# Optimization experiments

Measured on AMD Instinct MI355X. Metric: run time of the kernel, lower is better.

Reference implementation:

```python
import jax, jax.numpy as jnp
import numpy as np

B, T, D, H = 4, 2048, 1024, 16
HD = D // H  # 64
NEG = -np.finfo(np.float32).max


def setup_inputs() -> dict:
    key = jax.random.key(0)
    ks = jax.random.split(key, 9)
    s = 1.0 / np.sqrt(D)
    return {
        "x": jax.random.normal(ks[0], (B, T, D), jnp.float32),
        "wq": jax.random.normal(ks[1], (D, D), jnp.float32) * s,
        "bq": jax.random.normal(ks[2], (D,), jnp.float32) * 0.02,
        "wk": jax.random.normal(ks[3], (D, D), jnp.float32) * s,
        "bk": jax.random.normal(ks[4], (D,), jnp.float32) * 0.02,
        "wv": jax.random.normal(ks[5], (D, D), jnp.float32) * s,
        "bv": jax.random.normal(ks[6], (D,), jnp.float32) * 0.02,
        "wo": jax.random.normal(ks[7], (D, D), jnp.float32) * s,
        "bo": jax.random.normal(ks[8], (D,), jnp.float32) * 0.02,
    }


def reference(x, wq, bq, wk, bk, wv, bv, wo, bo):
    b, t, d = x.shape
    # separate Q, K, V projections, reshape to (B, H, T, HD)
    def proj(w, bias):
        y = x @ w + bias
        return y.reshape(b, t, H, HD).transpose(0, 2, 1, 3)
    q = proj(wq, bq)
    k = proj(wk, bk)
    v = proj(wv, bv)
    scale = 1.0 / np.sqrt(HD).astype(np.float32)
    scores = jnp.einsum("bhqd,bhkd->bhqk", q, k) * scale  # (B,H,T,T)
    # causal mask: -max_float on strictly upper triangle (matches source)
    mask = jnp.triu(jnp.full((t, t), NEG, jnp.float32), k=1)
    attn = jax.nn.softmax(scores + mask, axis=-1)
    out = jnp.einsum("bhqk,bhkd->bhqd", attn, v)
    out = out.transpose(0, 2, 1, 3).reshape(b, t, d)
    return out @ wo + bo
```

## Files before the change

kernel.cpp:

```cpp
#include <hip/hip_runtime.h>

typedef __bf16 bf16x8 __attribute__((ext_vector_type(8)));
typedef float f32x4 __attribute__((ext_vector_type(4)));

#define B_ 4
#define T_ 2048
#define D_ 1024
#define H_ 16
#define HD_ 64
#define M_ 8192
#define QSCALE 0.1803368801111204f

__device__ __forceinline__ ushort f2b(float f) {
  union { float f; unsigned u; } v; v.f = f;
  unsigned u = v.u;
  return (ushort)((u + 0x7FFFu + ((u >> 16) & 1u)) >> 16);
}

__device__ __forceinline__ unsigned pkbf(float a, float b) {
  union { float f; unsigned u; } va, vb; va.f = a; vb.f = b;
  return __builtin_amdgcn_perm(vb.u + 0x8000u, va.u + 0x8000u, 0x07060302u);
}

__device__ __forceinline__ void gll16(const void* g, void* l) {
  __builtin_amdgcn_global_load_lds(
      (const __attribute__((address_space(1))) unsigned*)g,
      (__attribute__((address_space(3))) unsigned*)l, 16, 0, 0);
}

__global__ __launch_bounds__(256) void cast_x_kernel(const float* __restrict__ x,
                                                     ushort* __restrict__ xb) {
  int idx = blockIdx.x * 256 + threadIdx.x;
  float4 v = ((const float4*)x)[idx];
  ushort4 o;
  o.x = f2b(v.x); o.y = f2b(v.y); o.z = f2b(v.z); o.w = f2b(v.w);
  ((ushort4*)xb)[idx] = o;
}

__global__ __launch_bounds__(256) void transpose_w_kernel(
    const float* __restrict__ wq, const float* __restrict__ wk,
    const float* __restrict__ wv, const float* __restrict__ wo,
    ushort* __restrict__ wt_qkv, ushort* __restrict__ wt_o) {
  __shared__ float tile[32][33];
  int z = blockIdx.z;
  const float* src = (z == 0) ? wq : (z == 1) ? wk : (z == 2) ? wv : wo;
  ushort* dst = (z < 3) ? (wt_qkv + (size_t)z * D_ * D_) : wt_o;
  int n0 = blockIdx.x * 32, k0 = blockIdx.y * 32;
  int tx = threadIdx.x & 31, ty = threadIdx.x >> 5;
  for (int i = 0; i < 4; i++) {
    int r = ty + i * 8;
    tile[r][tx] = src[(size_t)(k0 + r) * D_ + n0 + tx];
  }
  __syncthreads();
  for (int i = 0; i < 4; i++) {
    int r = ty + i * 8;
    dst[(size_t)(n0 + r) * D_ + k0 + tx] = f2b(tile[tx][r]);
  }
}

__global__ __launch_bounds__(256) void gemm_kernel(
    const ushort* __restrict__ A, const ushort* __restrict__ Bt, int mode,
    const float* __restrict__ bias_q, const float* __restrict__ bias_k,
    const float* __restrict__ bias_v,
    ushort* __restrict__ qb, ushort* __restrict__ kb, ushort* __restrict__ vtb,
    float* __restrict__ outf) {
  __shared__ ushort As[2][128][64];
  __shared__ ushort Bs[2][128][64];
  int tid = threadIdx.x;
  int wave = tid >> 6, lane = tid & 63, lrow = lane >> 4, lcol = lane & 15;
  int m0 = blockIdx.y * 128, n0 = blockIdx.x * 128;
  int wm = (wave & 1) * 64, wn = (wave >> 1) * 64;

  int rb = tid >> 3;
  int dc = tid & 7;
  int scv = dc ^ (rb & 7);
  const ushort* aBase = A + (size_t)(m0 + rb) * D_ + scv * 8;
  const ushort* bBase = Bt + (size_t)(n0 + rb) * D_ + scv * 8;

  f32x4 zero = {0.f, 0.f, 0.f, 0.f};
  f32x4 acc[4][4];
  for (int i = 0; i < 4; i++)
    for (int j = 0; j < 4; j++) acc[i][j] = zero;

  int swz = lcol & 7;

  auto stage = [&](int buf, int k) {
#pragma unroll
    for (int g = 0; g < 4; g++) {
      gll16(aBase + (size_t)(32 * g) * D_ + k, &As[buf][0][0] + tid * 8 + g * 2048);
      gll16(bBase + (size_t)(32 * g) * D_ + k, &Bs[buf][0][0] + tid * 8 + g * 2048);
    }
  };

  stage(0, 0);

  for (int k0 = 0; k0 < D_; k0 += 64) {
    int cur = (k0 >> 6) & 1, nxt = cur ^ 1;
    __syncthreads();
    if (k0 + 64 < D_) stage(nxt, k0 + 64);

    for (int ks = 0; ks < 2; ks++) {
      bf16x8 af[4], bf[4];
      int ch = ((ks * 4 + lrow) ^ swz) * 8;
      for (int mt = 0; mt < 4; mt++)
        af[mt] = *(const bf16x8*)&As[cur][wm + mt * 16 + lcol][ch];
      for (int nt = 0; nt < 4; nt++)
        bf[nt] = *(const bf16x8*)&Bs[cur][wn + nt * 16 + lcol][ch];
      for (int mt = 0; mt < 4; mt++)
        for (int nt = 0; nt < 4; nt++)
          acc[mt][nt] = __builtin_amdgcn_mfma_f32_16x16x32_bf16(
              af[mt], bf[nt], acc[mt][nt], 0, 0, 0);
    }
  }

  if (mode == 0) {
    int proj = n0 >> 10;
    const float* bias = (proj == 0) ? bias_q : (proj == 1) ? bias_k : bias_v;
    for (int mt = 0; mt < 4; mt++) {
      int gm0 = m0 + wm + mt * 16 + lrow * 4;
      int b = gm0 >> 11, tp = gm0 & 2047;
      for (int nt = 0; nt < 4; nt++) {
        int gn = n0 + wn + nt * 16 + lcol;
        int inner = gn & 1023;
        int h = inner >> 6, hd = inner & 63;
        float bv = bias[inner];
        if (proj == 0) {
          size_t base = ((size_t)(b * H_ + h) * T_ + tp) * HD_ + hd;
          for (int r = 0; r < 4; r++)
            qb[base + (size_t)r * HD_] = f2b((acc[mt][nt][r] + bv) * QSCALE);
        } else if (proj == 1) {
          size_t base = ((size_t)(b * H_ + h) * T_ + tp) * HD_ + hd;
          for (int r = 0; r < 4; r++)
            kb[base + (size_t)r * HD_] = f2b(acc[mt][nt][r] + bv);
        } else {
          ushort4 pk;
          pk.x = f2b(acc[mt][nt][0] + bv);
          pk.y = f2b(acc[mt][nt][1] + bv);
          pk.z = f2b(acc[mt][nt][2] + bv);
          pk.w = f2b(acc[mt][nt][3] + bv);
          *(ushort4*)&vtb[((size_t)(b * H_ + h) * HD_ + hd) * T_ + tp] = pk;
        }
      }
    }
  } else {
    for (int mt = 0; mt < 4; mt++) {
      int gm0 = m0 + wm + mt * 16 + lrow * 4;
      for (int nt = 0; nt < 4; nt++) {
        int gn = n0 + wn + nt * 16 + lcol;
        float bv = bias_q[gn];
        for (int r = 0; r < 4; r++)
          outf[(size_t)(gm0 + r) * D_ + gn] = acc[mt][nt][r] + bv;
      }
    }
  }
}

__global__ __launch_bounds__(256) void flash_kernel(
    const ushort* __restrict__ qb, const ushort* __restrict__ kb,
    const ushort* __restrict__ vtb, ushort* __restrict__ ob) {
  __shared__ ushort Ks[64][72];
  __shared__ ushort Vs[64][72];
  __shared__ ushort Ps[4][16][72];
  int tid = threadIdx.x;
  int wave = tid >> 6, lane = tid & 63, lrow = lane >> 4, lcol = lane & 15;

  int bid = blockIdx.x + (blockIdx.y << 5);
  int xcd = bid & 7;
  int slot = bid >> 3;
  int bh = xcd * 8 + (slot >> 5);
  int qtile = 31 - (slot & 31);
  int b = bh >> 4, h = bh & 15;
  const ushort* qh = qb + (size_t)bh * T_ * HD_;
  const ushort* kh = kb + (size_t)bh * T_ * HD_;
  const ushort* vh = vtb + (size_t)bh * HD_ * T_;

  int r0 = tid >> 3, cb0 = (tid & 7) * 8;
  uint4 kr0 = *(const uint4*)&kh[(size_t)r0 * HD_ + cb0];
  uint4 kr1 = *(const uint4*)&kh[(size_t)(r0 + 32) * HD_ + cb0];
  uint4 vr0 = *(const uint4*)&vh[(size_t)r0 * T_ + cb0];
  uint4 vr1 = *(const uint4*)&vh[(size_t)(r0 + 32) * T_ + cb0];

  bf16x8 af1;
  {
    __bf16 ov = (__bf16)((lcol == 0) ? 1.0f : 0.0f);
    for (int i = 0; i < 8; i++) af1[i] = ov;
  }

  f32x4 zero = {0.f, 0.f, 0.f, 0.f};

  int q0w = qtile * 64 + wave * 16;
  bf16x8 qf[2];
  for (int ks = 0; ks < 2; ks++)
    qf[ks] = *(const bf16x8*)&qh[(size_t)(q0w + lcol) * HD_ + ks * 32 + lrow * 8];

  f32x4 accO[4];
  f32x4 accI;
  accI = zero;
  for (int mt = 0; mt < 4; mt++) accO[mt] = zero;

  for (int j = 0; j <= qtile; j++) {
    __syncthreads();
    *(uint4*)&Ks[r0][cb0] = kr0;
    *(uint4*)&Ks[r0 + 32][cb0] = kr1;
    *(uint4*)&Vs[r0][cb0] = vr0;
    *(uint4*)&Vs[r0 + 32][cb0] = vr1;
    __syncthreads();

    if (j < qtile) {
      int jn = j + 1;
      kr0 = *(const uint4*)&kh[(size_t)(jn * 64 + r0) * HD_ + cb0];
      kr1 = *(const uint4*)&kh[(size_t)(jn * 64 + r0 + 32) * HD_ + cb0];
      vr0 = *(const uint4*)&vh[(size_t)r0 * T_ + jn * 64 + cb0];
      vr1 = *(const uint4*)&vh[(size_t)(r0 + 32) * T_ + jn * 64 + cb0];
    }

    f32x4 st[4];
    for (int mt = 0; mt < 4; mt++) st[mt] = zero;
    for (int ks = 0; ks < 2; ks++)
      for (int mt = 0; mt < 4; mt++) {
        bf16x8 kf = *(const bf16x8*)&Ks[mt * 16 + lcol][ks * 32 + lrow * 8];
        st[mt] = __builtin_amdgcn_mfma_f32_16x16x32_bf16(kf, qf[ks], st[mt], 0, 0, 0);
      }

    if (j == qtile) {
      int q_g = q0w + lcol;
      for (int mt = 0; mt < 4; mt++)
        for (int r = 0; r < 4; r++) {
          int kv_g = j * 64 + mt * 16 + lrow * 4 + r;
          if (kv_g > q_g) st[mt][r] = -1e30f;
        }
    }

    for (int mt = 0; mt < 4; mt++)
      for (int r = 0; r < 4; r++)
        st[mt][r] = __builtin_amdgcn_exp2f(st[mt][r]);

    for (int mt = 0; mt < 4; mt++) {
      uint2 pk;
      pk.x = pkbf(st[mt][0], st[mt][1]);
      pk.y = pkbf(st[mt][2], st[mt][3]);
      *(uint2*)&Ps[wave][lcol][mt * 16 + lrow * 4] = pk;
    }

    for (int ks = 0; ks < 2; ks++) {
      bf16x8 pf = *(const bf16x8*)&Ps[wave][lcol][ks * 32 + lrow * 8];
      accI = __builtin_amdgcn_mfma_f32_16x16x32_bf16(af1, pf, accI, 0, 0, 0);
      for (int mt = 0; mt < 4; mt++) {
        bf16x8 vf = *(const bf16x8*)&Vs[mt * 16 + lcol][ks * 32 + lrow * 8];
        accO[mt] = __builtin_amdgcn_mfma_f32_16x16x32_bf16(vf, pf, accO[mt], 0, 0, 0);
      }
    }
  }

  float lsum = __shfl(accI[0], lcol);
  float linv = 1.f / lsum;
  int t = q0w + lcol;
  size_t base = ((size_t)b * T_ + t) * D_ + h * HD_;
  for (int mt = 0; mt < 4; mt++) {
    uint2 pk;
    pk.x = pkbf(accO[mt][0] * linv, accO[mt][1] * linv);
    pk.y = pkbf(accO[mt][2] * linv, accO[mt][3] * linv);
    *(uint2*)&ob[base + mt * 16 + lrow * 4] = pk;
  }
}

extern "C" void kernel_launch(void* const* d_in, const int* in_sizes, int n_in,
                              void* d_out, int out_size, void* d_ws, size_t ws_size,
                              hipStream_t stream) {
  (void)in_sizes; (void)n_in; (void)out_size; (void)ws_size;
  const float* x  = (const float*)d_in[0];
  const float* wq = (const float*)d_in[1];
  const float* bq = (const float*)d_in[2];
  const float* wk = (const float*)d_in[3];
  const float* bk = (const float*)d_in[4];
  const float* wv = (const float*)d_in[5];
  const float* bv = (const float*)d_in[6];
  const float* wo = (const float*)d_in[7];
  const float* bo = (const float*)d_in[8];
  float* out = (float*)d_out;

  char* ws = (char*)d_ws;
  ushort* xb     = (ushort*)(ws);
  ushort* wt_qkv = (ushort*)(ws + 16777216);
  ushort* wt_o   = (ushort*)(ws + 23068672);
  ushort* qb     = (ushort*)(ws + 25165824);
  ushort* kb     = (ushort*)(ws + 41943040);
  ushort* vtb    = (ushort*)(ws + 58720256);
  ushort* ob     = (ushort*)(ws + 75497472);

  cast_x_kernel<<<8192, 256, 0, stream>>>(x, xb);
  transpose_w_kernel<<<dim3(32, 32, 4), 256, 0, stream>>>(wq, wk, wv, wo, wt_qkv, wt_o);
  gemm_kernel<<<dim3(24, 64), 256, 0, stream>>>(xb, wt_qkv, 0, bq, bk, bv, qb, kb, vtb, nullptr);
  flash_kernel<<<dim3(32, 64), 256, 0, stream>>>(qb, kb, vtb, ob);
  gemm_kernel<<<dim3(8, 64), 256, 0, stream>>>(ob, wt_o, 1, bo, nullptr, nullptr,
                                               nullptr, nullptr, nullptr, out);
}
```

Before: 268.1 us.

## Double flash query tile per block, add XCD-aware GEMM remap and MFMA priority

The flash kernel now handles 128 query rows per block, with each wave owning 32 rows in two 16-row halves. Every K/V tile loaded into LDS is therefore reused across twice as many queries, and the grid is halved. LDS row padding changes to 80 and s_setprio is raised around the MFMA sections. The GEMM kernel remaps block IDs so consecutive work tiles land on the same XCD, aiming for better L2 locality. The cost is more registers per thread, which may reduce occupancy, and coarser causal load balance.

```diff
diff --git a/kernel.cpp b/kernel.cpp
--- a/kernel.cpp
+++ b/kernel.cpp
@@ -68,7 +68,12 @@
   __shared__ ushort Bs[2][128][64];
   int tid = threadIdx.x;
   int wave = tid >> 6, lane = tid & 63, lrow = lane >> 4, lcol = lane & 15;
-  int m0 = blockIdx.y * 128, n0 = blockIdx.x * 128;
+
+  int gx = gridDim.x;
+  int nwg = gx * gridDim.y;
+  int orig = blockIdx.x + gx * blockIdx.y;
+  int work = (orig & 7) * (nwg >> 3) + (orig >> 3);
+  int m0 = (work / gx) * 128, n0 = (work % gx) * 128;
   int wm = (wave & 1) * 64, wn = (wave >> 1) * 64;
 
   int rb = tid >> 3;
@@ -158,19 +163,19 @@
 __global__ __launch_bounds__(256) void flash_kernel(
     const ushort* __restrict__ qb, const ushort* __restrict__ kb,
     const ushort* __restrict__ vtb, ushort* __restrict__ ob) {
-  __shared__ ushort Ks[64][72];
-  __shared__ ushort Vs[64][72];
-  __shared__ ushort Ps[4][16][72];
+  __shared__ ushort Ks[64][80];
+  __shared__ ushort Vs[64][80];
+  __shared__ ushort Ps[4][32][80];
   int tid = threadIdx.x;
   int wave = tid >> 6, lane = tid & 63, lrow = lane >> 4, lcol = lane & 15;
 
-  int bid = blockIdx.x + (blockIdx.y << 5);
+  int bid = blockIdx.x + (blockIdx.y << 4);
   int xcd = bid & 7;
   int slot = bid >> 3;
-  int bh = xcd * 8 + (slot >> 5);
-  int qtile = 31 - (slot & 31);
+  int bh = xcd * 8 + (slot >> 4);
+  int qblk = 15 - (slot & 15);
   int b = bh >> 4, h = bh & 15;
-  const ushort* qh = qb + (size_t)bh * T_ * HD_;
+  const ushort* qp = qb + (size_t)bh * T_ * HD_;
   const ushort* kh = kb + (size_t)bh * T_ * HD_;
   const ushort* vh = vtb + (size_t)bh * HD_ * T_;
 
@@ -188,17 +193,25 @@
 
   f32x4 zero = {0.f, 0.f, 0.f, 0.f};
 
-  int q0w = qtile * 64 + wave * 16;
-  bf16x8 qf[2];
-  for (int ks = 0; ks < 2; ks++)
-    qf[ks] = *(const bf16x8*)&qh[(size_t)(q0w + lcol) * HD_ + ks * 32 + lrow * 8];
-
-  f32x4 accO[4];
-  f32x4 accI;
-  accI = zero;
-  for (int mt = 0; mt < 4; mt++) accO[mt] = zero;
-
-  for (int j = 0; j <= qtile; j++) {
+  int q0w = qblk * 128 + wave * 32;
+  bf16x8 qf[2][2];
+#pragma unroll
+  for (int qh = 0; qh < 2; qh++)
+#pragma unroll
+    for (int ks = 0; ks < 2; ks++)
+      qf[qh][ks] = *(const bf16x8*)&qp[(size_t)(q0w + qh * 16 + lcol) * HD_ +
+                                       ks * 32 + lrow * 8];
+
+  f32x4 accO[2][4];
+  f32x4 accS[2];
+#pragma unroll
+  for (int qh = 0; qh < 2; qh++) {
+    accS[qh] = zero;
+    for (int mt = 0; mt < 4; mt++) accO[qh][mt] = zero;
+  }
+
+  int nj = qblk * 2 + 2;
+  for (int j = 0; j < nj; j++) {
     __syncthreads();
     *(uint4*)&Ks[r0][cb0] = kr0;
     *(uint4*)&Ks[r0 + 32][cb0] = kr1;
@@ -206,7 +219,7 @@
     *(uint4*)&Vs[r0 + 32][cb0] = vr1;
     __syncthreads();
 
-    if (j < qtile) {
+    if (j + 1 < nj) {
       int jn = j + 1;
       kr0 = *(const uint4*)&kh[(size_t)(jn * 64 + r0) * HD_ + cb0];
       kr1 = *(const uint4*)&kh[(size_t)(jn * 64 + r0 + 32) * HD_ + cb0];
@@ -214,53 +227,81 @@
       vr1 = *(const uint4*)&vh[(size_t)(r0 + 32) * T_ + jn * 64 + cb0];
     }
 
-    f32x4 st[4];
-    for (int mt = 0; mt < 4; mt++) st[mt] = zero;
+    if (j * 64 > q0w + 31) continue;
+
+    f32x4 st[2][4];
+#pragma unroll
+    for (int qh = 0; qh < 2; qh++)
+      for (int mt = 0; mt < 4; mt++) st[qh][mt] = zero;
+    __builtin_amdgcn_s_setprio(1);
+#pragma unroll
     for (int ks = 0; ks < 2; ks++)
+#pragma unroll
       for (int mt = 0; mt < 4; mt++) {
         bf16x8 kf = *(const bf16x8*)&Ks[mt * 16 + lcol][ks * 32 + lrow * 8];
-        st[mt] = __builtin_amdgcn_mfma_f32_16x16x32_bf16(kf, qf[ks], st[mt], 0, 0, 0);
-      }
-
-    if (j == qtile) {
-      int q_g = q0w + lcol;
+        st[0][mt] = __builtin_amdgcn_mfma_f32_16x16x32_bf16(kf, qf[0][ks], st[0][mt], 0, 0, 0);
+        st[1][mt] = __builtin_amdgcn_mfma_f32_16x16x32_bf16(kf, qf[1][ks], st[1][mt], 0, 0, 0);
+      }
+    __builtin_amdgcn_s_setprio(0);
+
+    if (j >= 2 * qblk) {
+#pragma unroll
+      for (int qh = 0; qh < 2; qh++) {
+        int q_g = q0w + qh * 16 + lcol;
+#pragma unroll
+        for (int mt = 0; mt < 4; mt++)
+          for (int r = 0; r < 4; r++) {
+            int kv_g = j * 64 + mt * 16 + lrow * 4 + r;
+            if (kv_g > q_g) st[qh][mt][r] = -1e30f;
+          }
+      }
+    }
+
+#pragma unroll
+    for (int qh = 0; qh < 2; qh++)
       for (int mt = 0; mt < 4; mt++)
-        for (int r = 0; r < 4; r++) {
-          int kv_g = j * 64 + mt * 16 + lrow * 4 + r;
-          if (kv_g > q_g) st[mt][r] = -1e30f;
-        }
-    }
-
-    for (int mt = 0; mt < 4; mt++)
-      for (int r = 0; r < 4; r++)
-        st[mt][r] = __builtin_amdgcn_exp2f(st[mt][r]);
-
+        for (int r = 0; r < 4; r++)
+          st[qh][mt][r] = __builtin_amdgcn_exp2f(st[qh][mt][r]);
+
+#pragma unroll
+    for (int qh = 0; qh < 2; qh++)
+      for (int mt = 0; mt < 4; mt++) {
+        uint2 pk;
+        pk.x = pkbf(st[qh][mt][0], st[qh][mt][1]);
+        pk.y = pkbf(st[qh][mt][2], st[qh][mt][3]);
+        *(uint2*)&Ps[wave][qh * 16 + lcol][mt * 16 + lrow * 4] = pk;
+      }
+
+    __builtin_amdgcn_s_setprio(1);
+#pragma unroll
+    for (int ks = 0; ks < 2; ks++) {
+      bf16x8 pf0 = *(const bf16x8*)&Ps[wave][lcol][ks * 32 + lrow * 8];
+      bf16x8 pf1 = *(const bf16x8*)&Ps[wave][16 + lcol][ks * 32 + lrow * 8];
+      accS[0] = __builtin_amdgcn_mfma_f32_16x16x32_bf16(af1, pf0, accS[0], 0, 0, 0);
+      accS[1] = __builtin_amdgcn_mfma_f32_16x16x32_bf16(af1, pf1, accS[1], 0, 0, 0);
+#pragma unroll
+      for (int mt = 0; mt < 4; mt++) {
+        bf16x8 vf = *(const bf16x8*)&Vs[mt * 16 + lcol][ks * 32 + lrow * 8];
+        accO[0][mt] = __builtin_amdgcn_mfma_f32_16x16x32_bf16(vf, pf0, accO[0][mt], 0, 0, 0);
+        accO[1][mt] = __builtin_amdgcn_mfma_f32_16x16x32_bf16(vf, pf1, accO[1][mt], 0, 0, 0);
+      }
+    }
+    __builtin_amdgcn_s_setprio(0);
+  }
+
+#pragma unroll
+  for (int qh = 0; qh < 2; qh++) {
+    float lsum = __shfl(accS[qh][0], lcol);
+    float linv = 1.f / lsum;
+    int t = q0w + qh * 16 + lcol;
+    size_t base = ((size_t)b * T_ + t) * D_ + h * HD_;
+#pragma unroll
     for (int mt = 0; mt < 4; mt++) {
       uint2 pk;
-      pk.x = pkbf(st[mt][0], st[mt][1]);
-      pk.y = pkbf(st[mt][2], st[mt][3]);
-      *(uint2*)&Ps[wave][lcol][mt * 16 + lrow * 4] = pk;
-    }
-
-    for (int ks = 0; ks < 2; ks++) {
-      bf16x8 pf = *(const bf16x8*)&Ps[wave][lcol][ks * 32 + lrow * 8];
-      accI = __builtin_amdgcn_mfma_f32_16x16x32_bf16(af1, pf, accI, 0, 0, 0);
-      for (int mt = 0; mt < 4; mt++) {
-        bf16x8 vf = *(const bf16x8*)&Vs[mt * 16 + lcol][ks * 32 + lrow * 8];
-        accO[mt] = __builtin_amdgcn_mfma_f32_16x16x32_bf16(vf, pf, accO[mt], 0, 0, 0);
-      }
-    }
-  }
-
-  float lsum = __shfl(accI[0], lcol);
-  float linv = 1.f / lsum;
-  int t = q0w + lcol;
-  size_t base = ((size_t)b * T_ + t) * D_ + h * HD_;
-  for (int mt = 0; mt < 4; mt++) {
-    uint2 pk;
-    pk.x = pkbf(accO[mt][0] * linv, accO[mt][1] * linv);
-    pk.y = pkbf(accO[mt][2] * linv, accO[mt][3] * linv);
-    *(uint2*)&ob[base + mt * 16 + lrow * 4] = pk;
+      pk.x = pkbf(accO[qh][mt][0] * linv, accO[qh][mt][1] * linv);
+      pk.y = pkbf(accO[qh][mt][2] * linv, accO[qh][mt][3] * linv);
+      *(uint2*)&ob[base + mt * 16 + lrow * 4] = pk;
+    }
   }
 }
 
@@ -291,7 +332,7 @@
   cast_x_kernel<<<8192, 256, 0, stream>>>(x, xb);
   transpose_w_kernel<<<dim3(32, 32, 4), 256, 0, stream>>>(wq, wk, wv, wo, wt_qkv, wt_o);
   gemm_kernel<<<dim3(24, 64), 256, 0, stream>>>(xb, wt_qkv, 0, bq, bk, bv, qb, kb, vtb, nullptr);
-  flash_kernel<<<dim3(32, 64), 256, 0, stream>>>(qb, kb, vtb, ob);
+  flash_kernel<<<dim3(16, 64), 256, 0, stream>>>(qb, kb, vtb, ob);
   gemm_kernel<<<dim3(8, 64), 256, 0, stream>>>(ob, wt_o, 1, bo, nullptr, nullptr,
                                                nullptr, nullptr, nullptr, out);
 }
```

New measurement: 270.4 us. No clear change (+0.9%).
